# Optimization experiments

Hardware: AMD Instinct MI355X
Metric: run time of the kernel (lower is better)

The kernel has to match this reference:

```python
import jax, jax.numpy as jnp
import numpy as np

HEADS = 8
IN_C = 256
MDL = 512
N = 4
L = 4096
NE = 65536  # avg degree 16


def setup_inputs() -> dict:
    key = jax.random.key(0)
    ks = jax.random.split(key, 14)
    f32 = jnp.float32
    s = 0.05
    return {
        "queries": jax.random.normal(ks[0], (N, L, IN_C), f32),
        "keys": jax.random.normal(ks[1], (N, L, IN_C), f32),
        "values": jax.random.normal(ks[2], (N, L, IN_C), f32),
        "adj": jax.random.randint(ks[3], (2, NE), 0, L, dtype=jnp.int32),
        "edge_pos_enc": jax.random.normal(ks[4], (N, HEADS, NE), f32),
        "Wq": jax.random.normal(ks[5], (IN_C, MDL), f32) * s,
        "bq": jnp.zeros((MDL,), f32),
        "Wk": jax.random.normal(ks[6], (IN_C, MDL), f32) * s,
        "bk": jnp.zeros((MDL,), f32),
        "Wv": jax.random.normal(ks[7], (IN_C, MDL), f32) * s,
        "bv": jnp.zeros((MDL,), f32),
        "Wo": jax.random.normal(ks[8], (MDL, MDL), f32) * s,
        "bo": jnp.zeros((MDL,), f32),
    }


def reference(queries, keys, values, adj, edge_pos_enc, Wq, bq, Wk, bk, Wv, bv, Wo, bo):
    n, l, _ = queries.shape
    h = HEADS
    e = MDL // h  # per-head dim
    temp = 1.0 / jnp.sqrt(jnp.asarray(e, queries.dtype))
    dst, src = adj[0], adj[1]

    def split(x):  # (n, l, mdl) -> (n*h, l, e)
        return x.reshape(n, l, h, e).transpose(0, 2, 1, 3).reshape(n * h, l, e)

    q = split(queries @ Wq + bq)
    k = split(keys @ Wk + bk)
    v = split(values @ Wv + bv)
    epe = edge_pos_enc.reshape(n * h, NE)

    def head(qh, kh, vh, eh):
        # qh,kh,vh: (l, e); eh: (Ne,)
        scores = temp * (jnp.sum(qh[dst] * kh[src], axis=-1) + eh)  # (Ne,)
        m = jax.ops.segment_max(scores, dst, num_segments=l)
        p = jnp.exp(scores - m[dst])
        z = jax.ops.segment_sum(p, dst, num_segments=l)
        alpha = p / z[dst]  # segment softmax keyed by dst (adj[0])
        return jax.ops.segment_sum(alpha[:, None] * vh[src], dst, num_segments=l)  # (l, e)

    out = jax.vmap(head)(q, k, v, epe)  # (n*h, l, e)
    out = out.reshape(n, h, l, e).transpose(0, 2, 1, 3).reshape(n, l, h * e)
    return out @ Wo + bo
```

## Files before the change

kernel.cpp:

```cpp
#include <hip/hip_runtime.h>
#include <hip/hip_bf16.h>
#include <math.h>
#include <stdint.h>

#define HEADS 8
#define IN_C  256
#define MDL   512
#define NB    4
#define LL    4096
#define NE    65536
#define EDIM  64
#define TEMP  0.125f

typedef __bf16 bf16x8 __attribute__((ext_vector_type(8)));
typedef float  f32x4  __attribute__((ext_vector_type(4)));
typedef short  short8 __attribute__((ext_vector_type(8)));

__device__ __forceinline__ void glds16(const void* g, void* l) {
    __builtin_amdgcn_global_load_lds(
        (const __attribute__((address_space(1))) void*)g,
        (__attribute__((address_space(3))) void*)l, 16, 0, 0);
}

template<int OUTBF>
__device__ __forceinline__ void gemm_body(
    const __hip_bfloat16* __restrict__ A, const __hip_bfloat16* __restrict__ Bt,
    const float* __restrict__ bias, float* __restrict__ Cf,
    __hip_bfloat16* __restrict__ Cb, int M, int N, int K,
    __hip_bfloat16* As, __hip_bfloat16* Bs)
{
    const int tid  = threadIdx.x;
    const int lane = tid & 63;
    const int w    = tid >> 6;
    const int wr   = w >> 1, wc = w & 1;
    const int bm   = blockIdx.y * 128, bn = blockIdx.x * 128;

    const int r0 = tid >> 2;
    const int c0 = (tid & 3) ^ (r0 & 3);
    const int r1 = (256 + tid) >> 2;
    const int c1 = ((256 + tid) & 3) ^ (r1 & 3);
    const __hip_bfloat16* gA0 = A  + (size_t)(bm + r0) * K + c0 * 8;
    const __hip_bfloat16* gA1 = A  + (size_t)(bm + r1) * K + c1 * 8;
    const __hip_bfloat16* gB0 = Bt + (size_t)(bn + r0) * K + c0 * 8;
    const __hip_bfloat16* gB1 = Bt + (size_t)(bn + r1) * K + c1 * 8;
    __hip_bfloat16* lA0 = As + (size_t)(w * 64) * 8;
    __hip_bfloat16* lA1 = As + (size_t)(256 + w * 64) * 8;
    __hip_bfloat16* lB0 = Bs + (size_t)(w * 64) * 8;
    __hip_bfloat16* lB1 = Bs + (size_t)(256 + w * 64) * 8;

    int fa[4], fb[4];
    #pragma unroll
    for (int i = 0; i < 4; i++) {
        int rA = wr * 64 + i * 16 + (lane & 15);
        fa[i] = rA * 32 + (((lane >> 4) ^ (rA & 3)) * 8);
        int rB = wc * 64 + i * 16 + (lane & 15);
        fb[i] = rB * 32 + (((lane >> 4) ^ (rB & 3)) * 8);
    }

    f32x4 acc[4][4] = {};

    for (int k0 = 0; k0 < K; k0 += 32) {
        glds16(gA0 + k0, lA0);
        glds16(gA1 + k0, lA1);
        glds16(gB0 + k0, lB0);
        glds16(gB1 + k0, lB1);
        __syncthreads();

        bf16x8 av[4], bv[4];
        #pragma unroll
        for (int i = 0; i < 4; i++) av[i] = *(const bf16x8*)(As + fa[i]);
        #pragma unroll
        for (int i = 0; i < 4; i++) bv[i] = *(const bf16x8*)(Bs + fb[i]);
        #pragma unroll
        for (int mi = 0; mi < 4; mi++)
            #pragma unroll
            for (int ni = 0; ni < 4; ni++)
                acc[mi][ni] = __builtin_amdgcn_mfma_f32_16x16x32_bf16(
                    av[mi], bv[ni], acc[mi][ni], 0, 0, 0);
        __syncthreads();
    }

    #pragma unroll
    for (int mi = 0; mi < 4; mi++) {
        int row = bm + wr * 64 + mi * 16 + (lane >> 4) * 4;
        #pragma unroll
        for (int ni = 0; ni < 4; ni++) {
            int col = bn + wc * 64 + ni * 16 + (lane & 15);
            float bb = bias[col];
            #pragma unroll
            for (int j = 0; j < 4; j++) {
                float vv = acc[mi][ni][j] + bb;
                if (OUTBF) Cb[(size_t)(row + j) * N + col] = __float2bfloat16(vv);
                else       Cf[(size_t)(row + j) * N + col] = vv;
            }
        }
    }
}

__global__ __launch_bounds__(256) void gemm_qkv(
    const __hip_bfloat16* __restrict__ A0, const __hip_bfloat16* __restrict__ A1,
    const __hip_bfloat16* __restrict__ A2,
    const __hip_bfloat16* __restrict__ B0, const __hip_bfloat16* __restrict__ B1,
    const __hip_bfloat16* __restrict__ B2,
    const float* __restrict__ b0, const float* __restrict__ b1,
    const float* __restrict__ b2,
    __hip_bfloat16* __restrict__ C0, __hip_bfloat16* __restrict__ C1,
    __hip_bfloat16* __restrict__ C2, int M, int N, int K)
{
    __shared__ __align__(16) __hip_bfloat16 As[128 * 32];
    __shared__ __align__(16) __hip_bfloat16 Bs[128 * 32];
    int z = blockIdx.z;
    const __hip_bfloat16* A  = (z == 0) ? A0 : (z == 1) ? A1 : A2;
    const __hip_bfloat16* Bt = (z == 0) ? B0 : (z == 1) ? B1 : B2;
    const float* bias        = (z == 0) ? b0 : (z == 1) ? b1 : b2;
    __hip_bfloat16* C        = (z == 0) ? C0 : (z == 1) ? C1 : C2;
    gemm_body<1>(A, Bt, bias, nullptr, C, M, N, K, As, Bs);
}

__global__ __launch_bounds__(256) void gemm_out(
    const __hip_bfloat16* __restrict__ A, const __hip_bfloat16* __restrict__ Bt,
    const float* __restrict__ bias, float* __restrict__ C, int M, int N, int K)
{
    __shared__ __align__(16) __hip_bfloat16 As[128 * 32];
    __shared__ __align__(16) __hip_bfloat16 Bs[128 * 32];
    gemm_body<0>(A, Bt, bias, C, nullptr, M, N, K, As, Bs);
}

__global__ void count_edges(const int* __restrict__ dst, int* __restrict__ counts, int ne) {
    int e = blockIdx.x * blockDim.x + threadIdx.x;
    if (e < ne) atomicAdd(&counts[dst[e]], 1);
}

__global__ __launch_bounds__(1024) void scan_offsets(
    const int* __restrict__ counts, int* __restrict__ offsets, int* __restrict__ cursor)
{
    __shared__ int wsum[16];
    const int tid  = threadIdx.x;
    const int lane = tid & 63;
    const int wid  = tid >> 6;

    int c[4];
    int base = tid * 4;
    int s = 0;
    #pragma unroll
    for (int i = 0; i < 4; i++) { c[i] = counts[base + i]; s += c[i]; }

    int v = s;
    #pragma unroll
    for (int off = 1; off < 64; off <<= 1) {
        int t = __shfl_up(v, off);
        if (lane >= off) v += t;
    }
    if (lane == 63) wsum[wid] = v;
    __syncthreads();
    if (wid == 0) {
        int wv = (lane < 16) ? wsum[lane] : 0;
        #pragma unroll
        for (int off = 1; off < 16; off <<= 1) {
            int t = __shfl_up(wv, off);
            if (lane >= off) wv += t;
        }
        if (lane < 16) wsum[lane] = wv;
    }
    __syncthreads();

    int prefix = (wid > 0 ? wsum[wid - 1] : 0) + (v - s);
    int run = prefix;
    #pragma unroll
    for (int i = 0; i < 4; i++) {
        offsets[base + i] = run;
        cursor[base + i]  = run;
        run += c[i];
    }
    if (tid == 1023) offsets[4096] = run;
}

#define N8 524288
__global__ __launch_bounds__(256) void prep(
    const int* __restrict__ dst, const int* __restrict__ srcarr,
    const float* __restrict__ epe, int* __restrict__ cursor,
    int* __restrict__ src_s, float* __restrict__ epe_s,
    const float* __restrict__ q, const float* __restrict__ k,
    const float* __restrict__ v,
    __hip_bfloat16* __restrict__ Qin, __hip_bfloat16* __restrict__ Kin,
    __hip_bfloat16* __restrict__ Vin,
    const float* __restrict__ Wq, const float* __restrict__ Wk,
    const float* __restrict__ Wv, const float* __restrict__ Wo,
    __hip_bfloat16* __restrict__ Wqt, __hip_bfloat16* __restrict__ Wkt,
    __hip_bfloat16* __restrict__ Wvt, __hip_bfloat16* __restrict__ Wot)
{
    __shared__ float t[32][33];
    const int b = blockIdx.x;

    if (b < 256) {
        int e = b * 256 + threadIdx.x;
        int p = atomicAdd(&cursor[dst[e]], 1);
        src_s[p] = srcarr[e];
        #pragma unroll
        for (int n = 0; n < NB; n++) {
            float4 a2, b2;
            const float* base = epe + (size_t)(n * HEADS) * NE + e;
            a2.x = base[0 * NE]; a2.y = base[1 * NE]; a2.z = base[2 * NE]; a2.w = base[3 * NE];
            b2.x = base[4 * NE]; b2.y = base[5 * NE]; b2.z = base[6 * NE]; b2.w = base[7 * NE];
            float* o = epe_s + ((size_t)n * NE + p) * 8;
            *(float4*)o       = a2;
            *(float4*)(o + 4) = b2;
        }
    } else if (b < 6400) {
        int i = (b - 256) * 256 + threadIdx.x;
        int which = i >> 19;
        int j = i & (N8 - 1);
        const float* x = (which == 0) ? q : (which == 1) ? k : v;
        __hip_bfloat16* y = (which == 0) ? Qin : (which == 1) ? Kin : Vin;
        const float4* xv = (const float4*)x;
        float4 a2 = xv[2 * j], b2 = xv[2 * j + 1];
        union { short8 v8; __hip_bfloat16 h[8]; } u;
        u.h[0] = __float2bfloat16(a2.x); u.h[1] = __float2bfloat16(a2.y);
        u.h[2] = __float2bfloat16(a2.z); u.h[3] = __float2bfloat16(a2.w);
        u.h[4] = __float2bfloat16(b2.x); u.h[5] = __float2bfloat16(b2.y);
        u.h[6] = __float2bfloat16(b2.z); u.h[7] = __float2bfloat16(b2.w);
        *(short8*)(y + (size_t)j * 8) = u.v8;
    } else {
        int bb = b - 6400;
        const float* W; __hip_bfloat16* Wt; int K, tt;
        if (bb < 384) {
            int m = bb >> 7; tt = bb & 127; K = IN_C;
            W  = (m == 0) ? Wq  : (m == 1) ? Wk  : Wv;
            Wt = (m == 0) ? Wqt : (m == 1) ? Wkt : Wvt;
        } else {
            tt = bb - 384; K = MDL; W = Wo; Wt = Wot;
        }
        const int N = MDL;
        int bx = (tt & 15) * 32;
        int by = (tt >> 4) * 32;
        int tx = threadIdx.x & 31, ty = threadIdx.x >> 5;
        #pragma unroll
        for (int i = 0; i < 4; i++)
            t[ty + i * 8][tx] = W[(size_t)(by + ty + i * 8) * N + bx + tx];
        __syncthreads();
        #pragma unroll
        for (int i = 0; i < 4; i++)
            Wt[(size_t)(bx + ty + i * 8) * K + by + tx] =
                __float2bfloat16(t[tx][ty + i * 8]);
    }
}

__global__ __launch_bounds__(256) void sparse_attn6(
    const __hip_bfloat16* __restrict__ Qb, const __hip_bfloat16* __restrict__ Kb,
    const __hip_bfloat16* __restrict__ Vb,
    const int* __restrict__ src_s, const float* __restrict__ epe_s,
    const int* __restrict__ offsets, __hip_bfloat16* __restrict__ O)
{
    const int lane = threadIdx.x & 63;
    const int wid  = threadIdx.x >> 6;
    const int bid  = blockIdx.x;
    const int xcd  = bid & 7;
    const int n    = xcd >> 1;
    const int base = ((bid >> 3) << 1) | (xcd & 1);
    const int dstn = (base << 2) | wid;
    const int task = n * LL + dstn;
    const int hg   = lane >> 3;

    const size_t rowbase = (size_t)task * MDL;
    const int beg = offsets[dstn];
    const int end = offsets[dstn + 1];
    const int deg = end - beg;

    union { short8 v8; __hip_bfloat16 h[8]; } uo;
    if (deg == 0) {
        #pragma unroll
        for (int j = 0; j < 8; j++) uo.h[j] = __float2bfloat16(0.0f);
        *(short8*)(O + rowbase + lane * 8) = uo.v8;
        return;
    }

    bf16x8 q8 = *(const bf16x8*)(Qb + rowbase + lane * 8);
    float qf[8];
    #pragma unroll
    for (int j = 0; j < 8; j++) qf[j] = (float)q8[j];

    const __hip_bfloat16* Kn = Kb + (size_t)n * LL * MDL + lane * 8;
    const __hip_bfloat16* Vn = Vb + (size_t)n * LL * MDL + lane * 8;
    const float* pe_n = epe_s + (size_t)n * NE * 8 + hg;

    float acc[8] = {};

    if (deg <= 64) {
        const int my_src = src_s[beg + ((lane < deg) ? lane : (deg - 1))];

        float m = -INFINITY, z = 0.0f;
        float s_st[8];

        #pragma unroll
        for (int slot = 0; slot < 8; slot++) {
            const int r0 = slot * 8;
            if (r0 < deg) {
                bf16x8 kk[8];
                #pragma unroll
                for (int j = 0; j < 8; j++) {
                    int s = __shfl(my_src, r0 + j);
                    kk[j] = *(const bf16x8*)(Kn + (size_t)s * MDL);
                }
                const int rel_mine = r0 + (lane & 7);
                float pp = (rel_mine < deg)
                         ? pe_n[(size_t)(beg + rel_mine) * 8] : -INFINITY;

                float p[8];
                #pragma unroll
                for (int j = 0; j < 8; j++) {
                    float d = 0.0f;
                    #pragma unroll
                    for (int dd = 0; dd < 8; dd++)
                        d = fmaf(qf[dd], (float)kk[j][dd], d);
                    p[j] = d;
                }
                float n0, n1, n2, n3, u0, u1, sraw;
                {
                    float a0 = (lane & 1) ? p[1] : p[0];
                    float b0 = (lane & 1) ? p[0] : p[1];
                    n0 = a0 + __shfl_xor(b0, 1);
                    float a1 = (lane & 1) ? p[3] : p[2];
                    float b1 = (lane & 1) ? p[2] : p[3];
                    n1 = a1 + __shfl_xor(b1, 1);
                    float a2 = (lane & 1) ? p[5] : p[4];
                    float b2 = (lane & 1) ? p[4] : p[5];
                    n2 = a2 + __shfl_xor(b2, 1);
                    float a3 = (lane & 1) ? p[7] : p[6];
                    float b3 = (lane & 1) ? p[6] : p[7];
                    n3 = a3 + __shfl_xor(b3, 1);

                    float c0 = (lane & 2) ? n1 : n0;
                    float d0 = (lane & 2) ? n0 : n1;
                    u0 = c0 + __shfl_xor(d0, 2);
                    float c1 = (lane & 2) ? n3 : n2;
                    float d1 = (lane & 2) ? n2 : n3;
                    u1 = c1 + __shfl_xor(d1, 2);

                    float e0 = (lane & 4) ? u1 : u0;
                    float f0 = (lane & 4) ? u0 : u1;
                    sraw = e0 + __shfl_xor(f0, 4);
                }

                float sc_my = TEMP * (sraw + pp);
                s_st[slot] = sc_my;

                float gm = sc_my;
                gm = fmaxf(gm, __shfl_xor(gm, 1));
                gm = fmaxf(gm, __shfl_xor(gm, 2));
                gm = fmaxf(gm, __shfl_xor(gm, 4));
                float mnew = fmaxf(m, gm);
                float e_my = __expf(sc_my - mnew);
                float gs = e_my;
                gs += __shfl_xor(gs, 1);
                gs += __shfl_xor(gs, 2);
                gs += __shfl_xor(gs, 4);
                z = z * __expf(m - mnew) + gs;
                m = mnew;
            } else {
                s_st[slot] = -INFINITY;
            }
        }

        const float zinv = 1.0f / z;
        float a_st[8];
        #pragma unroll
        for (int slot = 0; slot < 8; slot++)
            a_st[slot] = __expf(s_st[slot] - m) * zinv;

        #pragma unroll
        for (int slot = 0; slot < 8; slot++) {
            const int r0 = slot * 8;
            if (r0 < deg) {
                bf16x8 vv[8];
                #pragma unroll
                for (int j = 0; j < 8; j++) {
                    int s = __shfl(my_src, r0 + j);
                    vv[j] = *(const bf16x8*)(Vn + (size_t)s * MDL);
                }
                #pragma unroll
                for (int j = 0; j < 8; j++) {
                    float al = __shfl(a_st[slot], (lane & 56) | j);
                    #pragma unroll
                    for (int dd = 0; dd < 8; dd++)
                        acc[dd] = fmaf(al, (float)vv[j][dd], acc[dd]);
                }
            }
        }
    } else {
        float m = -INFINITY, z = 0.0f;
        bf16x8 ka[4], va[4], kb2[4], vb2[4];
        float  pa[4], pb2[4];

        #define LOADB(i, kk, vv, pp)                                        \
            _Pragma("unroll")                                               \
            for (int j = 0; j < 4; j++) {                                   \
                int idx = (i) + j;                                          \
                int ok  = idx < end;                                        \
                int s   = ok ? src_s[idx] : src_s[beg];                     \
                size_t rk = (size_t)s * MDL;                                \
                kk[j] = *(const bf16x8*)(Kn + rk);                          \
                vv[j] = *(const bf16x8*)(Vn + rk);                          \
                pp[j] = ok ? pe_n[(size_t)idx * 8] : -INFINITY;             \
            }

        #define COMPUTE(kk, vv, pp)                                         \
        {                                                                   \
            float sc4[4];                                                   \
            _Pragma("unroll")                                               \
            for (int j = 0; j < 4; j++) {                                   \
                float d = 0.0f;                                             \
                _Pragma("unroll")                                           \
                for (int dd = 0; dd < 8; dd++) d += qf[dd] * (float)kk[j][dd]; \
                d += __shfl_xor(d, 1);                                      \
                d += __shfl_xor(d, 2);                                      \
                d += __shfl_xor(d, 4);                                      \
                sc4[j] = TEMP * (d + pp[j]);                                \
            }                                                               \
            float mb   = fmaxf(fmaxf(sc4[0], sc4[1]), fmaxf(sc4[2], sc4[3])); \
            float mnew = fmaxf(m, mb);                                      \
            float sc   = __expf(m - mnew);                                  \
            float pe0 = __expf(sc4[0] - mnew);                              \
            float pe1 = __expf(sc4[1] - mnew);                              \
            float pe2 = __expf(sc4[2] - mnew);                              \
            float pe3 = __expf(sc4[3] - mnew);                              \
            z = z * sc + (pe0 + pe1 + pe2 + pe3);                           \
            _Pragma("unroll")                                               \
            for (int dd = 0; dd < 8; dd++) {                                \
                float tt = acc[dd] * sc;                                    \
                tt = fmaf(pe0, (float)vv[0][dd], tt);                       \
                tt = fmaf(pe1, (float)vv[1][dd], tt);                       \
                tt = fmaf(pe2, (float)vv[2][dd], tt);                       \
                tt = fmaf(pe3, (float)vv[3][dd], tt);                       \
                acc[dd] = tt;                                               \
            }                                                               \
            m = mnew;                                                       \
        }

        LOADB(beg, ka, va, pa)
        for (int i = beg; i < end; i += 4) {
            if (i + 4 < end) { LOADB(i + 4, kb2, vb2, pb2) }
            COMPUTE(ka, va, pa)
            #pragma unroll
            for (int j = 0; j < 4; j++) { ka[j] = kb2[j]; va[j] = vb2[j]; pa[j] = pb2[j]; }
        }
        float inv = 1.0f / z;
        #pragma unroll
        for (int dd = 0; dd < 8; dd++) acc[dd] *= inv;
        #undef LOADB
        #undef COMPUTE
    }

    #pragma unroll
    for (int j = 0; j < 8; j++) uo.h[j] = __float2bfloat16(acc[j]);
    *(short8*)(O + rowbase + lane * 8) = uo.v8;
}

extern "C" void kernel_launch(void* const* d_in, const int* in_sizes, int n_in,
                              void* d_out, int out_size, void* d_ws, size_t ws_size,
                              hipStream_t stream)
{
    const float* queries = (const float*)d_in[0];
    const float* keys    = (const float*)d_in[1];
    const float* values  = (const float*)d_in[2];
    const int*   adj     = (const int*)d_in[3];
    const float* epe     = (const float*)d_in[4];
    const float* Wq = (const float*)d_in[5];
    const float* bq = (const float*)d_in[6];
    const float* Wk = (const float*)d_in[7];
    const float* bk = (const float*)d_in[8];
    const float* Wv = (const float*)d_in[9];
    const float* bv = (const float*)d_in[10];
    const float* Wo = (const float*)d_in[11];
    const float* bo = (const float*)d_in[12];
    float* out = (float*)d_out;

    const int* dst = adj;
    const int* src = adj + NE;

    const int    M   = NB * LL;
    const size_t NLM = (size_t)M * MDL;
    const size_t NLK = (size_t)M * IN_C;

    char* w = (char*)d_ws;
    __hip_bfloat16* Qb  = (__hip_bfloat16*)w; w += NLM * 2;
    __hip_bfloat16* Kb  = (__hip_bfloat16*)w; w += NLM * 2;
    __hip_bfloat16* Vb  = (__hip_bfloat16*)w; w += NLM * 2;
    char* inbf_base = w;
    __hip_bfloat16* Qin = (__hip_bfloat16*)w; w += NLK * 2;
    __hip_bfloat16* Kin = (__hip_bfloat16*)w; w += NLK * 2;
    __hip_bfloat16* Vin = (__hip_bfloat16*)w; w += NLK * 2;
    __hip_bfloat16* Ob  = (__hip_bfloat16*)inbf_base;
    __hip_bfloat16* Wqt = (__hip_bfloat16*)w; w += (size_t)MDL * IN_C * 2;
    __hip_bfloat16* Wkt = (__hip_bfloat16*)w; w += (size_t)MDL * IN_C * 2;
    __hip_bfloat16* Wvt = (__hip_bfloat16*)w; w += (size_t)MDL * IN_C * 2;
    __hip_bfloat16* Wot = (__hip_bfloat16*)w; w += (size_t)MDL * MDL * 2;
    int* counts  = (int*)w; w += 4096 * sizeof(int);
    int* offsets = (int*)w; w += 4100 * sizeof(int);
    int* cursor  = (int*)w; w += 4096 * sizeof(int);
    int*   src_s = (int*)w; w += NE * sizeof(int);
    float* epe_s = (float*)w; w += (size_t)NB * NE * 8 * sizeof(float);

    hipMemsetAsync(counts, 0, 4096 * sizeof(int), stream);
    count_edges<<<NE / 256, 256, 0, stream>>>(dst, counts, NE);
    scan_offsets<<<1, 1024, 0, stream>>>(counts, offsets, cursor);

    prep<<<7040, 256, 0, stream>>>(dst, src, epe, cursor, src_s, epe_s,
                                   queries, keys, values, Qin, Kin, Vin,
                                   Wq, Wk, Wv, Wo, Wqt, Wkt, Wvt, Wot);

    dim3 g3(MDL / 128, M / 128, 3);
    gemm_qkv<<<g3, 256, 0, stream>>>(Qin, Kin, Vin, Wqt, Wkt, Wvt, bq, bk, bv,
                                     Qb, Kb, Vb, M, MDL, IN_C);

    sparse_attn6<<<(NB * LL) / 4, 256, 0, stream>>>(Qb, Kb, Vb, src_s, epe_s, offsets, Ob);

    dim3 g(MDL / 128, M / 128);
    gemm_out<<<g, 256, 0, stream>>>(Ob, Wot, bo, out, M, MDL, MDL);
}
```

Baseline: 140.2 us.

## Fuse input bf16 cast into QKV GEMM, degree-sort attention rows, widen out-GEMM K tile

The QKV GEMM now reads the fp32 inputs directly and converts them to bf16 while staging into LDS. This drops the separate cast pass in prep and its intermediate buffers. The scan kernel buckets destination nodes by degree and writes a reorder table, so attention blocks process rows of similar degree together to reduce wave imbalance. The output GEMM moves to a K tile of 64 with an 8-way swizzle, halving the barrier count per K step at the cost of more LDS.

```diff
diff --git a/kernel.cpp b/kernel.cpp
--- a/kernel.cpp
+++ b/kernel.cpp
@@ -22,84 +22,18 @@
         (__attribute__((address_space(3))) void*)l, 16, 0, 0);
 }
 
-template<int OUTBF>
-__device__ __forceinline__ void gemm_body(
-    const __hip_bfloat16* __restrict__ A, const __hip_bfloat16* __restrict__ Bt,
-    const float* __restrict__ bias, float* __restrict__ Cf,
-    __hip_bfloat16* __restrict__ Cb, int M, int N, int K,
-    __hip_bfloat16* As, __hip_bfloat16* Bs)
-{
-    const int tid  = threadIdx.x;
-    const int lane = tid & 63;
-    const int w    = tid >> 6;
-    const int wr   = w >> 1, wc = w & 1;
-    const int bm   = blockIdx.y * 128, bn = blockIdx.x * 128;
-
-    const int r0 = tid >> 2;
-    const int c0 = (tid & 3) ^ (r0 & 3);
-    const int r1 = (256 + tid) >> 2;
-    const int c1 = ((256 + tid) & 3) ^ (r1 & 3);
-    const __hip_bfloat16* gA0 = A  + (size_t)(bm + r0) * K + c0 * 8;
-    const __hip_bfloat16* gA1 = A  + (size_t)(bm + r1) * K + c1 * 8;
-    const __hip_bfloat16* gB0 = Bt + (size_t)(bn + r0) * K + c0 * 8;
-    const __hip_bfloat16* gB1 = Bt + (size_t)(bn + r1) * K + c1 * 8;
-    __hip_bfloat16* lA0 = As + (size_t)(w * 64) * 8;
-    __hip_bfloat16* lA1 = As + (size_t)(256 + w * 64) * 8;
-    __hip_bfloat16* lB0 = Bs + (size_t)(w * 64) * 8;
-    __hip_bfloat16* lB1 = Bs + (size_t)(256 + w * 64) * 8;
-
-    int fa[4], fb[4];
-    #pragma unroll
-    for (int i = 0; i < 4; i++) {
-        int rA = wr * 64 + i * 16 + (lane & 15);
-        fa[i] = rA * 32 + (((lane >> 4) ^ (rA & 3)) * 8);
-        int rB = wc * 64 + i * 16 + (lane & 15);
-        fb[i] = rB * 32 + (((lane >> 4) ^ (rB & 3)) * 8);
-    }
-
-    f32x4 acc[4][4] = {};
-
-    for (int k0 = 0; k0 < K; k0 += 32) {
-        glds16(gA0 + k0, lA0);
-        glds16(gA1 + k0, lA1);
-        glds16(gB0 + k0, lB0);
-        glds16(gB1 + k0, lB1);
-        __syncthreads();
-
-        bf16x8 av[4], bv[4];
-        #pragma unroll
-        for (int i = 0; i < 4; i++) av[i] = *(const bf16x8*)(As + fa[i]);
-        #pragma unroll
-        for (int i = 0; i < 4; i++) bv[i] = *(const bf16x8*)(Bs + fb[i]);
-        #pragma unroll
-        for (int mi = 0; mi < 4; mi++)
-            #pragma unroll
-            for (int ni = 0; ni < 4; ni++)
-                acc[mi][ni] = __builtin_amdgcn_mfma_f32_16x16x32_bf16(
-                    av[mi], bv[ni], acc[mi][ni], 0, 0, 0);
-        __syncthreads();
-    }
-
-    #pragma unroll
-    for (int mi = 0; mi < 4; mi++) {
-        int row = bm + wr * 64 + mi * 16 + (lane >> 4) * 4;
-        #pragma unroll
-        for (int ni = 0; ni < 4; ni++) {
-            int col = bn + wc * 64 + ni * 16 + (lane & 15);
-            float bb = bias[col];
-            #pragma unroll
-            for (int j = 0; j < 4; j++) {
-                float vv = acc[mi][ni][j] + bb;
-                if (OUTBF) Cb[(size_t)(row + j) * N + col] = __float2bfloat16(vv);
-                else       Cf[(size_t)(row + j) * N + col] = vv;
-            }
-        }
-    }
+__device__ __forceinline__ short8 cvt8(float4 a, float4 b) {
+    union { short8 v; __hip_bfloat16 h[8]; } u;
+    u.h[0] = __float2bfloat16(a.x); u.h[1] = __float2bfloat16(a.y);
+    u.h[2] = __float2bfloat16(a.z); u.h[3] = __float2bfloat16(a.w);
+    u.h[4] = __float2bfloat16(b.x); u.h[5] = __float2bfloat16(b.y);
+    u.h[6] = __float2bfloat16(b.z); u.h[7] = __float2bfloat16(b.w);
+    return u.v;
 }
 
 __global__ __launch_bounds__(256) void gemm_qkv(
-    const __hip_bfloat16* __restrict__ A0, const __hip_bfloat16* __restrict__ A1,
-    const __hip_bfloat16* __restrict__ A2,
+    const float* __restrict__ A0, const float* __restrict__ A1,
+    const float* __restrict__ A2,
     const __hip_bfloat16* __restrict__ B0, const __hip_bfloat16* __restrict__ B1,
     const __hip_bfloat16* __restrict__ B2,
     const float* __restrict__ b0, const float* __restrict__ b1,
@@ -109,21 +43,165 @@
 {
     __shared__ __align__(16) __hip_bfloat16 As[128 * 32];
     __shared__ __align__(16) __hip_bfloat16 Bs[128 * 32];
-    int z = blockIdx.z;
-    const __hip_bfloat16* A  = (z == 0) ? A0 : (z == 1) ? A1 : A2;
+
+    const int z = blockIdx.z;
+    const float* A           = (z == 0) ? A0 : (z == 1) ? A1 : A2;
     const __hip_bfloat16* Bt = (z == 0) ? B0 : (z == 1) ? B1 : B2;
     const float* bias        = (z == 0) ? b0 : (z == 1) ? b1 : b2;
     __hip_bfloat16* C        = (z == 0) ? C0 : (z == 1) ? C1 : C2;
-    gemm_body<1>(A, Bt, bias, nullptr, C, M, N, K, As, Bs);
+
+    const int tid  = threadIdx.x;
+    const int lane = tid & 63;
+    const int w    = tid >> 6;
+    const int wr   = w >> 1, wc = w & 1;
+    const int bm   = blockIdx.y * 128, bn = blockIdx.x * 128;
+
+    const int r0  = tid >> 2;
+    const int cc0 = tid & 3;
+    const int ca0 = cc0 ^ (r0 & 3);
+    const int r1  = r0 + 64;
+    const int ca1 = cc0 ^ (r1 & 3);
+    const float* gA0 = A + (size_t)(bm + r0) * K + ca0 * 8;
+    const float* gA1 = A + (size_t)(bm + r1) * K + ca1 * 8;
+    __hip_bfloat16* lA0w = As + r0 * 32 + cc0 * 8;
+    __hip_bfloat16* lA1w = As + r1 * 32 + cc0 * 8;
+
+    const int cb0 = (tid & 3) ^ (r0 & 3);
+    const int cb1 = (tid & 3) ^ (r1 & 3);
+    const __hip_bfloat16* gB0 = Bt + (size_t)(bn + r0) * K + cb0 * 8;
+    const __hip_bfloat16* gB1 = Bt + (size_t)(bn + r1) * K + cb1 * 8;
+    __hip_bfloat16* lB0 = Bs + (size_t)(w * 64) * 8;
+    __hip_bfloat16* lB1 = Bs + (size_t)(256 + w * 64) * 8;
+
+    int fa[4], fb[4];
+    #pragma unroll
+    for (int i = 0; i < 4; i++) {
+        int rA = wr * 64 + i * 16 + (lane & 15);
+        fa[i] = rA * 32 + (((lane >> 4) ^ (rA & 3)) * 8);
+        int rB = wc * 64 + i * 16 + (lane & 15);
+        fb[i] = rB * 32 + (((lane >> 4) ^ (rB & 3)) * 8);
+    }
+
+    f32x4 acc[4][4] = {};
+
+    for (int k0 = 0; k0 < K; k0 += 32) {
+        glds16(gB0 + k0, lB0);
+        glds16(gB1 + k0, lB1);
+        float4 a0  = *(const float4*)(gA0 + k0);
+        float4 a0b = *(const float4*)(gA0 + k0 + 4);
+        float4 a1  = *(const float4*)(gA1 + k0);
+        float4 a1b = *(const float4*)(gA1 + k0 + 4);
+        *(short8*)lA0w = cvt8(a0, a0b);
+        *(short8*)lA1w = cvt8(a1, a1b);
+        __syncthreads();
+
+        bf16x8 av[4], bv[4];
+        #pragma unroll
+        for (int i = 0; i < 4; i++) av[i] = *(const bf16x8*)(As + fa[i]);
+        #pragma unroll
+        for (int i = 0; i < 4; i++) bv[i] = *(const bf16x8*)(Bs + fb[i]);
+        #pragma unroll
+        for (int mi = 0; mi < 4; mi++)
+            #pragma unroll
+            for (int ni = 0; ni < 4; ni++)
+                acc[mi][ni] = __builtin_amdgcn_mfma_f32_16x16x32_bf16(
+                    av[mi], bv[ni], acc[mi][ni], 0, 0, 0);
+        __syncthreads();
+    }
+
+    #pragma unroll
+    for (int mi = 0; mi < 4; mi++) {
+        int row = bm + wr * 64 + mi * 16 + (lane >> 4) * 4;
+        #pragma unroll
+        for (int ni = 0; ni < 4; ni++) {
+            int col = bn + wc * 64 + ni * 16 + (lane & 15);
+            float bb = bias[col];
+            #pragma unroll
+            for (int j = 0; j < 4; j++)
+                C[(size_t)(row + j) * N + col] = __float2bfloat16(acc[mi][ni][j] + bb);
+        }
+    }
 }
 
 __global__ __launch_bounds__(256) void gemm_out(
     const __hip_bfloat16* __restrict__ A, const __hip_bfloat16* __restrict__ Bt,
     const float* __restrict__ bias, float* __restrict__ C, int M, int N, int K)
 {
-    __shared__ __align__(16) __hip_bfloat16 As[128 * 32];
-    __shared__ __align__(16) __hip_bfloat16 Bs[128 * 32];
-    gemm_body<0>(A, Bt, bias, C, nullptr, M, N, K, As, Bs);
+    __shared__ __align__(16) __hip_bfloat16 As[128 * 64];
+    __shared__ __align__(16) __hip_bfloat16 Bs[128 * 64];
+
+    const int tid  = threadIdx.x;
+    const int lane = tid & 63;
+    const int w    = tid >> 6;
+    const int wr   = w >> 1, wc = w & 1;
+    const int bm   = blockIdx.y * 128, bn = blockIdx.x * 128;
+
+    const __hip_bfloat16* gA[4];
+    const __hip_bfloat16* gB[4];
+    __hip_bfloat16* lA[4];
+    __hip_bfloat16* lB[4];
+    #pragma unroll
+    for (int it = 0; it < 4; it++) {
+        int idx = it * 256 + tid;
+        int r = idx >> 3;
+        int c = (idx & 7) ^ (r & 7);
+        gA[it] = A  + (size_t)(bm + r) * K + c * 8;
+        gB[it] = Bt + (size_t)(bn + r) * K + c * 8;
+        lA[it] = As + (size_t)(it * 256 + w * 64) * 8;
+        lB[it] = Bs + (size_t)(it * 256 + w * 64) * 8;
+    }
+
+    int fa[2][4], fb[2][4];
+    #pragma unroll
+    for (int kk = 0; kk < 2; kk++)
+        #pragma unroll
+        for (int i = 0; i < 4; i++) {
+            int rA = wr * 64 + i * 16 + (lane & 15);
+            int gc = kk * 4 + (lane >> 4);
+            fa[kk][i] = rA * 64 + (gc ^ (rA & 7)) * 8;
+            int rB = wc * 64 + i * 16 + (lane & 15);
+            fb[kk][i] = rB * 64 + (gc ^ (rB & 7)) * 8;
+        }
+
+    f32x4 acc[4][4] = {};
+
+    for (int k0 = 0; k0 < K; k0 += 64) {
+        #pragma unroll
+        for (int it = 0; it < 4; it++) {
+            glds16(gA[it] + k0, lA[it]);
+            glds16(gB[it] + k0, lB[it]);
+        }
+        __syncthreads();
+
+        #pragma unroll
+        for (int kk = 0; kk < 2; kk++) {
+            bf16x8 av[4], bv[4];
+            #pragma unroll
+            for (int i = 0; i < 4; i++) av[i] = *(const bf16x8*)(As + fa[kk][i]);
+            #pragma unroll
+            for (int i = 0; i < 4; i++) bv[i] = *(const bf16x8*)(Bs + fb[kk][i]);
+            #pragma unroll
+            for (int mi = 0; mi < 4; mi++)
+                #pragma unroll
+                for (int ni = 0; ni < 4; ni++)
+                    acc[mi][ni] = __builtin_amdgcn_mfma_f32_16x16x32_bf16(
+                        av[mi], bv[ni], acc[mi][ni], 0, 0, 0);
+        }
+        __syncthreads();
+    }
+
+    #pragma unroll
+    for (int mi = 0; mi < 4; mi++) {
+        int row = bm + wr * 64 + mi * 16 + (lane >> 4) * 4;
+        #pragma unroll
+        for (int ni = 0; ni < 4; ni++) {
+            int col = bn + wc * 64 + ni * 16 + (lane & 15);
+            float bb = bias[col];
+            #pragma unroll
+            for (int j = 0; j < 4; j++)
+                C[(size_t)(row + j) * N + col] = acc[mi][ni][j] + bb;
+        }
+    }
 }
 
 __global__ void count_edges(const int* __restrict__ dst, int* __restrict__ counts, int ne) {
@@ -132,12 +210,16 @@
 }
 
 __global__ __launch_bounds__(1024) void scan_offsets(
-    const int* __restrict__ counts, int* __restrict__ offsets, int* __restrict__ cursor)
+    const int* __restrict__ counts, int* __restrict__ offsets,
+    int* __restrict__ cursor, int* __restrict__ reorder)
 {
     __shared__ int wsum[16];
+    __shared__ int bcnt[9], boff[9];
     const int tid  = threadIdx.x;
     const int lane = tid & 63;
     const int wid  = tid >> 6;
+
+    if (tid < 9) bcnt[tid] = 0;
 
     int c[4];
     int base = tid * 4;
@@ -166,24 +248,35 @@
 
     int prefix = (wid > 0 ? wsum[wid - 1] : 0) + (v - s);
     int run = prefix;
+    int mybk[4];
     #pragma unroll
     for (int i = 0; i < 4; i++) {
         offsets[base + i] = run;
         cursor[base + i]  = run;
         run += c[i];
+        int sc = (c[i] + 7) >> 3; if (sc > 8) sc = 8;
+        mybk[i] = 8 - sc;
+        atomicAdd(&bcnt[mybk[i]], 1);
     }
     if (tid == 1023) offsets[4096] = run;
-}
-
-#define N8 524288
+    __syncthreads();
+    if (tid == 0) {
+        int acc0 = 0;
+        #pragma unroll
+        for (int b = 0; b < 9; b++) { boff[b] = acc0; acc0 += bcnt[b]; }
+    }
+    __syncthreads();
+    #pragma unroll
+    for (int i = 0; i < 4; i++) {
+        int pos = atomicAdd(&boff[mybk[i]], 1);
+        reorder[pos] = base + i;
+    }
+}
+
 __global__ __launch_bounds__(256) void prep(
     const int* __restrict__ dst, const int* __restrict__ srcarr,
     const float* __restrict__ epe, int* __restrict__ cursor,
     int* __restrict__ src_s, float* __restrict__ epe_s,
-    const float* __restrict__ q, const float* __restrict__ k,
-    const float* __restrict__ v,
-    __hip_bfloat16* __restrict__ Qin, __hip_bfloat16* __restrict__ Kin,
-    __hip_bfloat16* __restrict__ Vin,
     const float* __restrict__ Wq, const float* __restrict__ Wk,
     const float* __restrict__ Wv, const float* __restrict__ Wo,
     __hip_bfloat16* __restrict__ Wqt, __hip_bfloat16* __restrict__ Wkt,
@@ -206,22 +299,8 @@
             *(float4*)o       = a2;
             *(float4*)(o + 4) = b2;
         }
-    } else if (b < 6400) {
-        int i = (b - 256) * 256 + threadIdx.x;
-        int which = i >> 19;
-        int j = i & (N8 - 1);
-        const float* x = (which == 0) ? q : (which == 1) ? k : v;
-        __hip_bfloat16* y = (which == 0) ? Qin : (which == 1) ? Kin : Vin;
-        const float4* xv = (const float4*)x;
-        float4 a2 = xv[2 * j], b2 = xv[2 * j + 1];
-        union { short8 v8; __hip_bfloat16 h[8]; } u;
-        u.h[0] = __float2bfloat16(a2.x); u.h[1] = __float2bfloat16(a2.y);
-        u.h[2] = __float2bfloat16(a2.z); u.h[3] = __float2bfloat16(a2.w);
-        u.h[4] = __float2bfloat16(b2.x); u.h[5] = __float2bfloat16(b2.y);
-        u.h[6] = __float2bfloat16(b2.z); u.h[7] = __float2bfloat16(b2.w);
-        *(short8*)(y + (size_t)j * 8) = u.v8;
     } else {
-        int bb = b - 6400;
+        int bb = b - 256;
         const float* W; __hip_bfloat16* Wt; int K, tt;
         if (bb < 384) {
             int m = bb >> 7; tt = bb & 127; K = IN_C;
@@ -245,11 +324,12 @@
     }
 }
 
-__global__ __launch_bounds__(256) void sparse_attn6(
+__global__ __launch_bounds__(256) void sparse_attn7(
     const __hip_bfloat16* __restrict__ Qb, const __hip_bfloat16* __restrict__ Kb,
     const __hip_bfloat16* __restrict__ Vb,
     const int* __restrict__ src_s, const float* __restrict__ epe_s,
-    const int* __restrict__ offsets, __hip_bfloat16* __restrict__ O)
+    const int* __restrict__ offsets, const int* __restrict__ reorder,
+    __hip_bfloat16* __restrict__ O)
 {
     const int lane = threadIdx.x & 63;
     const int wid  = threadIdx.x >> 6;
@@ -257,7 +337,7 @@
     const int xcd  = bid & 7;
     const int n    = xcd >> 1;
     const int base = ((bid >> 3) << 1) | (xcd & 1);
-    const int dstn = (base << 2) | wid;
+    const int dstn = reorder[(base << 2) | wid];
     const int task = n * LL + dstn;
     const int hg   = lane >> 3;
 
@@ -479,17 +559,12 @@
 
     const int    M   = NB * LL;
     const size_t NLM = (size_t)M * MDL;
-    const size_t NLK = (size_t)M * IN_C;
 
     char* w = (char*)d_ws;
     __hip_bfloat16* Qb  = (__hip_bfloat16*)w; w += NLM * 2;
     __hip_bfloat16* Kb  = (__hip_bfloat16*)w; w += NLM * 2;
     __hip_bfloat16* Vb  = (__hip_bfloat16*)w; w += NLM * 2;
-    char* inbf_base = w;
-    __hip_bfloat16* Qin = (__hip_bfloat16*)w; w += NLK * 2;
-    __hip_bfloat16* Kin = (__hip_bfloat16*)w; w += NLK * 2;
-    __hip_bfloat16* Vin = (__hip_bfloat16*)w; w += NLK * 2;
-    __hip_bfloat16* Ob  = (__hip_bfloat16*)inbf_base;
+    __hip_bfloat16* Ob  = (__hip_bfloat16*)w; w += NLM * 2;
     __hip_bfloat16* Wqt = (__hip_bfloat16*)w; w += (size_t)MDL * IN_C * 2;
     __hip_bfloat16* Wkt = (__hip_bfloat16*)w; w += (size_t)MDL * IN_C * 2;
     __hip_bfloat16* Wvt = (__hip_bfloat16*)w; w += (size_t)MDL * IN_C * 2;
@@ -497,22 +572,23 @@
     int* counts  = (int*)w; w += 4096 * sizeof(int);
     int* offsets = (int*)w; w += 4100 * sizeof(int);
     int* cursor  = (int*)w; w += 4096 * sizeof(int);
+    int* reorder = (int*)w; w += 4096 * sizeof(int);
     int*   src_s = (int*)w; w += NE * sizeof(int);
     float* epe_s = (float*)w; w += (size_t)NB * NE * 8 * sizeof(float);
 
     hipMemsetAsync(counts, 0, 4096 * sizeof(int), stream);
     count_edges<<<NE / 256, 256, 0, stream>>>(dst, counts, NE);
-    scan_offsets<<<1, 1024, 0, stream>>>(counts, offsets, cursor);
-
-    prep<<<7040, 256, 0, stream>>>(dst, src, epe, cursor, src_s, epe_s,
-                                   queries, keys, values, Qin, Kin, Vin,
-                                   Wq, Wk, Wv, Wo, Wqt, Wkt, Wvt, Wot);
+    scan_offsets<<<1, 1024, 0, stream>>>(counts, offsets, cursor, reorder);
+
+    prep<<<896, 256, 0, stream>>>(dst, src, epe, cursor, src_s, epe_s,
+                                  Wq, Wk, Wv, Wo, Wqt, Wkt, Wvt, Wot);
 
     dim3 g3(MDL / 128, M / 128, 3);
-    gemm_qkv<<<g3, 256, 0, stream>>>(Qin, Kin, Vin, Wqt, Wkt, Wvt, bq, bk, bv,
-                                     Qb, Kb, Vb, M, MDL, IN_C);
-
-    sparse_attn6<<<(NB * LL) / 4, 256, 0, stream>>>(Qb, Kb, Vb, src_s, epe_s, offsets, Ob);
+    gemm_qkv<<<g3, 256, 0, stream>>>(queries, keys, values, Wqt, Wkt, Wvt,
+                                     bq, bk, bv, Qb, Kb, Vb, M, MDL, IN_C);
+
+    sparse_attn7<<<(NB * LL) / 4, 256, 0, stream>>>(Qb, Kb, Vb, src_s, epe_s,
+                                                    offsets, reorder, Ob);
 
     dim3 g(MDL / 128, M / 128);
     gemm_out<<<g, 256, 0, stream>>>(Ob, Wot, bo, out, M, MDL, MDL);
```

After: 138.3 us. About the same (-1.3%).
